# Performance work log

Measured on AMD Instinct MI355X. Metric: run time of the kernel, lower is better.

The kernel has to match this reference:

```python
import jax, jax.numpy as jnp
import numpy as np

B, T, C, FFN, N_LAYER, LAYER_ID = 4, 2048, 1024, 4096, 24, 1
EPS = 1e-5


def setup_inputs() -> dict:
    key = jax.random.key(0)
    ks = jax.random.split(key, 10)
    scale = 0.02

    def w(k, shape):
        return (jax.random.normal(k, shape, jnp.float32) * scale)

    # RWKV-4 init formulas for layer_id=1, n_layer=24 (learned params, init per source)
    r01 = LAYER_ID / (N_LAYER - 1)
    r10 = 1.0 - LAYER_ID / N_LAYER
    ddd = np.arange(C, dtype=np.float64) / C
    h = np.arange(C, dtype=np.float64)
    decay = -5.0 + 8.0 * (h / (C - 1)) ** (0.7 + 1.3 * r01)
    zigzag = np.array([(i + 1) % 3 - 1 for i in range(C)], dtype=np.float64) * 0.5
    tfirst = np.log(0.3) + zigzag

    return {
        "x": jax.random.normal(ks[0], (B, T, C), jnp.float32),
        "ln1_w": jnp.ones((C,), jnp.float32), "ln1_b": jnp.zeros((C,), jnp.float32),
        "ln2_w": jnp.ones((C,), jnp.float32), "ln2_b": jnp.zeros((C,), jnp.float32),
        "time_decay": jnp.asarray(decay, jnp.float32),
        "time_first": jnp.asarray(tfirst, jnp.float32),
        "tmk": jnp.asarray(ddd ** r10, jnp.float32),
        "tmv": jnp.asarray(ddd ** r10 + 0.3 * r01, jnp.float32),
        "tmr": jnp.asarray(ddd ** (0.5 * r10), jnp.float32),
        "att_kw": w(ks[1], (C, C)), "att_vw": w(ks[2], (C, C)),
        "att_rw": w(ks[3], (C, C)), "att_ow": w(ks[4], (C, C)),
        "f_tmk": jnp.asarray(ddd ** r10, jnp.float32),
        "f_tmr": jnp.asarray(ddd ** r10, jnp.float32),
        "f_kw": w(ks[5], (FFN, C)), "f_rw": w(ks[6], (C, C)), "f_vw": w(ks[7], (C, FFN)),
    }


def _ln(z, g, b):
    m = jnp.mean(z, axis=-1, keepdims=True)
    v = jnp.mean(jnp.square(z - m), axis=-1, keepdims=True)
    return (z - m) * jax.lax.rsqrt(v + EPS) * g + b


def _shift(z):  # token shift: prepend zero row along T, drop last
    return jnp.pad(z, ((0, 0), (1, 0), (0, 0)))[:, :-1]


def _wkv(time_decay, u, k, v):
    # Numerically-stable RWKV-4 WKV recurrence (log-space max trick).
    # k, v: [B, T, C]; time_decay, u: [C]
    w = -jnp.exp(time_decay)  # per-channel decay (negative)
    kt = jnp.moveaxis(k, 1, 0)  # [T, B, C]
    vt = jnp.moveaxis(v, 1, 0)
    aa = jnp.zeros_like(kt[0])
    bb = jnp.zeros_like(kt[0])
    pp = jnp.full_like(kt[0], -1e38)

    def step(carry, kv):
        aa, bb, pp = carry
        kk, vv = kv
        ww = u + kk
        p = jnp.maximum(pp, ww)
        e1 = jnp.exp(pp - p)
        e2 = jnp.exp(ww - p)
        out = (e1 * aa + e2 * vv) / (e1 * bb + e2)
        ww2 = pp + w
        p2 = jnp.maximum(ww2, kk)
        e1b = jnp.exp(ww2 - p2)
        e2b = jnp.exp(kk - p2)
        return (e1b * aa + e2b * vv, e1b * bb + e2b, p2), out

    _, out = jax.lax.scan(step, (aa, bb, pp), (kt, vt))
    return jnp.moveaxis(out, 0, 1)  # [B, T, C]


def reference(x, ln1_w, ln1_b, ln2_w, ln2_b, time_decay, time_first,
              tmk, tmv, tmr, att_kw, att_vw, att_rw, att_ow,
              f_tmk, f_tmr, f_kw, f_rw, f_vw):
    # --- RWKV_TimeMix (layer_id != 0; protectors are identity in fwd for finite vals) ---
    h = _ln(x, ln1_w, ln1_b)
    hx = _shift(h)
    xk = h * tmk + hx * (1.0 - tmk)
    xv = h * tmv + hx * (1.0 - tmv)
    xr = h * tmr + hx * (1.0 - tmr)
    k = jnp.einsum('btc,dc->btd', xk, att_kw)
    v = jnp.einsum('btc,dc->btd', xv, att_vw)
    sr = jax.nn.sigmoid(jnp.einsum('btc,dc->btd', xr, att_rw))
    rwkv = sr * _wkv(time_decay, time_first, k, v)
    x = x + jnp.einsum('btd,cd->btc', rwkv, att_ow)
    # --- RWKV_ChannelMix ---
    h = _ln(x, ln2_w, ln2_b)
    hx = _shift(h)
    xk = h * f_tmk + hx * (1.0 - f_tmk)
    xr = h * f_tmr + hx * (1.0 - f_tmr)
    kk = jnp.square(jax.nn.relu(jnp.einsum('btc,fc->btf', xk, f_kw)))
    kv = jnp.einsum('btf,cf->btc', kk, f_vw)
    x = x + jax.nn.sigmoid(jnp.einsum('btc,dc->btd', xr, f_rw)) * kv
    return x
```

## Files before the change

kernel.cpp:

```cpp
#include <hip/hip_runtime.h>
#include <cstdint>

#define C_DIM 1024
#define T_DIM 2048
#define B_DIM 4
#define FFN_DIM 4096
#define NROWS (B_DIM * T_DIM)
#define NELEM ((size_t)NROWS * C_DIM)
#define MB ((size_t)1 << 20)
#define NSEG 32
#define SEGL (T_DIM / NSEG)

typedef __bf16 bf16;
typedef __bf16 bf16x4 __attribute__((ext_vector_type(4)));
typedef __bf16 bf16x8 __attribute__((ext_vector_type(8)));
typedef float  floatx4 __attribute__((ext_vector_type(4)));

#define GLDS(g, l) __builtin_amdgcn_global_load_lds(                          \
    (const __attribute__((address_space(1))) void*)(g),                       \
    (__attribute__((address_space(3))) void*)(l), 16, 0, 0)

__device__ __forceinline__ void store_out(float* p, float v) { *p = v; }
__device__ __forceinline__ void store_out(bf16* p, float v)  { *p = (bf16)v; }

struct W7 {
    const float* s[7];
    bf16*        d[7];
    int          cum[8];
};

__global__ __launch_bounds__(256) void f2b7_kernel(W7 w)
{
    int id = blockIdx.x * 256 + threadIdx.x;
    int seg = 0;
#pragma unroll
    for (int j = 1; j < 7; ++j) if (id >= w.cum[j]) seg = j;
    int i = id - w.cum[seg];
    float4 v = ((const float4*)w.s[seg])[i];
    bf16x4 o = { (bf16)v.x, (bf16)v.y, (bf16)v.z, (bf16)v.w };
    ((bf16x4*)w.d[seg])[i] = o;
}

template<bool HASV>
__global__ __launch_bounds__(256) void lnmix_kernel(const float* __restrict__ x,
                                                    const float* __restrict__ g,
                                                    const float* __restrict__ b,
                                                    const float* __restrict__ mk,
                                                    const float* __restrict__ mv,
                                                    const float* __restrict__ mr,
                                                    bf16* __restrict__ xk,
                                                    bf16* __restrict__ xv,
                                                    bf16* __restrict__ xr)
{
    int row = blockIdx.x;
    int t   = row & (T_DIM - 1);
    int tid = threadIdx.x;
    size_t i4 = (size_t)row * 256 + tid;

    float4 v  = ((const float4*)x)[i4];
    float4 vp = make_float4(0.f, 0.f, 0.f, 0.f);
    if (t != 0) vp = ((const float4*)x)[i4 - 256];

    float s   = v.x + v.y + v.z + v.w;
    float s2  = v.x * v.x + v.y * v.y + v.z * v.z + v.w * v.w;
    float sp  = vp.x + vp.y + vp.z + vp.w;
    float sp2 = vp.x * vp.x + vp.y * vp.y + vp.z * vp.z + vp.w * vp.w;
    for (int off = 32; off > 0; off >>= 1) {
        s   += __shfl_down(s,   off);
        s2  += __shfl_down(s2,  off);
        sp  += __shfl_down(sp,  off);
        sp2 += __shfl_down(sp2, off);
    }
    __shared__ float red[16];
    int lane = tid & 63, wid = tid >> 6;
    if (lane == 0) { red[wid] = s; red[4 + wid] = s2; red[8 + wid] = sp; red[12 + wid] = sp2; }
    __syncthreads();
    s   = red[0] + red[1] + red[2] + red[3];
    s2  = red[4] + red[5] + red[6] + red[7];
    sp  = red[8] + red[9] + red[10] + red[11];
    sp2 = red[12] + red[13] + red[14] + red[15];

    float mean  = s * (1.0f / C_DIM);
    float inv   = rsqrtf(s2 * (1.0f / C_DIM) - mean * mean + 1e-5f);
    float meanp = sp * (1.0f / C_DIM);
    float invp  = rsqrtf(sp2 * (1.0f / C_DIM) - meanp * meanp + 1e-5f);

    float4 gv = ((const float4*)g)[tid];
    float4 bv = ((const float4*)b)[tid];
    float4 hv, hp;
    hv.x = (v.x - mean) * inv * gv.x + bv.x;
    hv.y = (v.y - mean) * inv * gv.y + bv.y;
    hv.z = (v.z - mean) * inv * gv.z + bv.z;
    hv.w = (v.w - mean) * inv * gv.w + bv.w;
    if (t != 0) {
        hp.x = (vp.x - meanp) * invp * gv.x + bv.x;
        hp.y = (vp.y - meanp) * invp * gv.y + bv.y;
        hp.z = (vp.z - meanp) * invp * gv.z + bv.z;
        hp.w = (vp.w - meanp) * invp * gv.w + bv.w;
    } else {
        hp = make_float4(0.f, 0.f, 0.f, 0.f);
    }

    float4 m1 = ((const float4*)mk)[tid];
    bf16x4 o;
    o.x = (bf16)(hp.x + m1.x * (hv.x - hp.x));
    o.y = (bf16)(hp.y + m1.y * (hv.y - hp.y));
    o.z = (bf16)(hp.z + m1.z * (hv.z - hp.z));
    o.w = (bf16)(hp.w + m1.w * (hv.w - hp.w));
    ((bf16x4*)xk)[i4] = o;

    if (HASV) {
        float4 m2 = ((const float4*)mv)[tid];
        o.x = (bf16)(hp.x + m2.x * (hv.x - hp.x));
        o.y = (bf16)(hp.y + m2.y * (hv.y - hp.y));
        o.z = (bf16)(hp.z + m2.z * (hv.z - hp.z));
        o.w = (bf16)(hp.w + m2.w * (hv.w - hp.w));
        ((bf16x4*)xv)[i4] = o;
    }

    float4 m3 = ((const float4*)mr)[tid];
    o.x = (bf16)(hp.x + m3.x * (hv.x - hp.x));
    o.y = (bf16)(hp.y + m3.y * (hv.y - hp.y));
    o.z = (bf16)(hp.z + m3.z * (hv.z - hp.z));
    o.w = (bf16)(hp.w + m3.w * (hv.w - hp.w));
    ((bf16x4*)xr)[i4] = o;
}

#define EPI_NONE 0
#define EPI_SIG 1
#define EPI_RELU2 2
#define EPI_ADD 3
#define EPI_SCALEADD 4

template<int EPI, typename OutT>
__global__ __launch_bounds__(256) void gemm_bf16(const bf16* __restrict__ A,
                                                 const bf16* __restrict__ W,
                                                 OutT* __restrict__ Y,
                                                 const float* __restrict__ X2,
                                                 const bf16* __restrict__ S,
                                                 int N, int K)
{
    __shared__ unsigned short As[128 * 32];
    __shared__ unsigned short Bs[128 * 32];

    int tid = threadIdx.x;
    int ntn    = N >> 7;
    int stride = ntn >> 3;
    int id  = blockIdx.x;
    int sq  = id >> 3;
    int n_t = (id & 7) * stride + (sq % stride);
    int m_t = sq / stride;
    int m0 = m_t * 128, n0 = n_t * 128;

    int r0  = tid >> 2;
    int qsw = ((tid & 3) - ((r0 >> 1) & 3)) & 3;
    const bf16* Ag = A + (size_t)(m0 + r0) * K + qsw * 8;
    const bf16* Wg = W + (size_t)(n0 + r0) * K + qsw * 8;
    size_t rowK = (size_t)64 * K;
    int wv = tid >> 6;
    unsigned short* AsW0 = As + wv * 512;
    unsigned short* AsW1 = As + 2048 + wv * 512;
    unsigned short* BsW0 = Bs + wv * 512;
    unsigned short* BsW1 = Bs + 2048 + wv * 512;

    int ln = tid & 63;
    int wm = (wv & 1) * 64, wn = (wv >> 1) * 64;
    int ra0 = wm + (ln & 15);
    int rb0 = wn + (ln & 15);
    int qa  = ln >> 4;
    int abase = ra0 * 32 + (((qa + (ra0 >> 1)) & 3) * 8);
    int bbase = rb0 * 32 + (((qa + (rb0 >> 1)) & 3) * 8);

    floatx4 acc[4][4] = {};

    for (int k0 = 0; k0 < K; k0 += 32) {
        if (k0) __syncthreads();
        GLDS(Ag + k0,        AsW0);
        GLDS(Ag + k0 + rowK, AsW1);
        GLDS(Wg + k0,        BsW0);
        GLDS(Wg + k0 + rowK, BsW1);
        __syncthreads();

        bf16x8 a[4], b[4];
#pragma unroll
        for (int i = 0; i < 4; ++i) a[i] = *(const bf16x8*)(As + abase + i * 512);
#pragma unroll
        for (int j = 0; j < 4; ++j) b[j] = *(const bf16x8*)(Bs + bbase + j * 512);
#pragma unroll
        for (int i = 0; i < 4; ++i)
#pragma unroll
            for (int j = 0; j < 4; ++j)
                acc[i][j] = __builtin_amdgcn_mfma_f32_16x16x32_bf16(a[i], b[j], acc[i][j], 0, 0, 0);
    }

    int row0 = (ln >> 4) * 4;
    int colb = n0 + wn + (ln & 15);
#pragma unroll
    for (int i = 0; i < 4; ++i) {
        int gm = m0 + wm + i * 16 + row0;
#pragma unroll
        for (int j = 0; j < 4; ++j) {
            int gn = colb + j * 16;
#pragma unroll
            for (int r = 0; r < 4; ++r) {
                size_t idx = (size_t)(gm + r) * N + gn;
                float v = acc[i][j][r];
                if (EPI == EPI_SIG)        v = 1.0f / (1.0f + __expf(-v));
                else if (EPI == EPI_RELU2) { float t = fmaxf(v, 0.0f); v = t * t; }
                else if (EPI == EPI_ADD)   v = X2[idx] + v;
                else if (EPI == EPI_SCALEADD) v = X2[idx] + (float)S[idx] * v;
                store_out(&Y[idx], v);
            }
        }
    }
}

__global__ __launch_bounds__(256) void wkv_seg(const float* __restrict__ k,
                                               const float* __restrict__ v,
                                               const float* __restrict__ decay,
                                               float* __restrict__ sa,
                                               float* __restrict__ sb,
                                               float* __restrict__ sp)
{
    int idx = blockIdx.x * 256 + threadIdx.x;
    int c   = idx & (C_DIM - 1);
    int bs  = idx >> 10;
    int seg = bs & (NSEG - 1);
    int b   = bs >> 5;
    float w = -__expf(decay[c]);
    size_t base = ((size_t)b * T_DIM + (size_t)seg * SEGL) * C_DIM + c;
    float aa = 0.f, bb = 0.f, pp = -1e38f;
    for (int t = 0; t < SEGL; ++t) {
        size_t off = base + (size_t)t * C_DIM;
        float kk = k[off], vv = v[off];
        float ww2 = pp + w;
        float p2  = fmaxf(ww2, kk);
        float e1  = __expf(ww2 - p2);
        float e2  = __expf(kk - p2);
        aa = e1 * aa + e2 * vv;
        bb = e1 * bb + e2;
        pp = p2;
    }
    sa[idx] = aa; sb[idx] = bb; sp[idx] = pp;
}

__global__ __launch_bounds__(256) void wkv_comb(const float* __restrict__ sa,
                                                const float* __restrict__ sb,
                                                const float* __restrict__ sp,
                                                const float* __restrict__ decay,
                                                float* __restrict__ ia,
                                                float* __restrict__ ib,
                                                float* __restrict__ ip)
{
    int idx = blockIdx.x * 256 + threadIdx.x;
    int c = idx & (C_DIM - 1);
    int b = idx >> 10;
    float wL = -__expf(decay[c]) * (float)SEGL;
    float aa = 0.f, bb = 0.f, pp = -1e38f;
    size_t base = (size_t)b * NSEG * C_DIM + c;
    for (int j = 0; j < NSEG; ++j) {
        size_t o = base + (size_t)j * C_DIM;
        ia[o] = aa; ib[o] = bb; ip[o] = pp;
        float a_s = sa[o], b_s = sb[o], p_s = sp[o];
        float pd = pp + wL;
        float pn = fmaxf(pd, p_s);
        float e1 = __expf(pd - pn);
        float e2 = __expf(p_s - pn);
        aa = e1 * aa + e2 * a_s;
        bb = e1 * bb + e2 * b_s;
        pp = pn;
    }
}

__global__ __launch_bounds__(256) void wkv_out(const float* __restrict__ k,
                                               const float* __restrict__ v,
                                               const bf16* __restrict__ sr,
                                               const float* __restrict__ decay,
                                               const float* __restrict__ first,
                                               const float* __restrict__ ia,
                                               const float* __restrict__ ib,
                                               const float* __restrict__ ip,
                                               bf16* __restrict__ out)
{
    int idx = blockIdx.x * 256 + threadIdx.x;
    int c   = idx & (C_DIM - 1);
    int bs  = idx >> 10;
    int seg = bs & (NSEG - 1);
    int b   = bs >> 5;
    float w = -__expf(decay[c]);
    float u = first[c];
    float aa = ia[idx], bb = ib[idx], pp = ip[idx];
    size_t base = ((size_t)b * T_DIM + (size_t)seg * SEGL) * C_DIM + c;
    for (int t = 0; t < SEGL; ++t) {
        size_t off = base + (size_t)t * C_DIM;
        float kk = k[off], vv = v[off];
        float ww = u + kk;
        float p  = fmaxf(pp, ww);
        float e1 = __expf(pp - p);
        float e2 = __expf(ww - p);
        float o  = (e1 * aa + e2 * vv) / (e1 * bb + e2);
        out[off] = (bf16)((float)sr[off] * o);
        float ww2 = pp + w;
        float p2  = fmaxf(ww2, kk);
        float e1b = __expf(ww2 - p2);
        float e2b = __expf(kk - p2);
        aa = e1b * aa + e2b * vv;
        bb = e1b * bb + e2b;
        pp = p2;
    }
}

extern "C" void kernel_launch(void* const* d_in, const int* in_sizes, int n_in,
                              void* d_out, int out_size, void* d_ws, size_t ws_size,
                              hipStream_t stream)
{
    const float* x          = (const float*)d_in[0];
    const float* ln1_w      = (const float*)d_in[1];
    const float* ln1_b      = (const float*)d_in[2];
    const float* ln2_w      = (const float*)d_in[3];
    const float* ln2_b      = (const float*)d_in[4];
    const float* time_decay = (const float*)d_in[5];
    const float* time_first = (const float*)d_in[6];
    const float* tmk        = (const float*)d_in[7];
    const float* tmv        = (const float*)d_in[8];
    const float* tmr        = (const float*)d_in[9];
    const float* att_kw     = (const float*)d_in[10];
    const float* att_vw     = (const float*)d_in[11];
    const float* att_rw     = (const float*)d_in[12];
    const float* att_ow     = (const float*)d_in[13];
    const float* f_tmk      = (const float*)d_in[14];
    const float* f_tmr      = (const float*)d_in[15];
    const float* f_kw       = (const float*)d_in[16];
    const float* f_rw       = (const float*)d_in[17];
    const float* f_vw       = (const float*)d_in[18];
    float* out = (float*)d_out;

    char* W8 = (char*)d_ws;
    bf16* kw_b  = (bf16*)(W8 + 0 * MB);
    bf16* vw_b  = (bf16*)(W8 + 2 * MB);
    bf16* rw_b  = (bf16*)(W8 + 4 * MB);
    bf16* ow_b  = (bf16*)(W8 + 6 * MB);
    bf16* fkw_b = (bf16*)(W8 + 8 * MB);
    bf16* frw_b = (bf16*)(W8 + 16 * MB);
    bf16* fvw_b = (bf16*)(W8 + 18 * MB);

    bf16*  xk_b   = (bf16*)(W8 + 26 * MB);
    bf16*  xv_b   = (bf16*)(W8 + 42 * MB);
    bf16*  xr_b   = (bf16*)(W8 + 58 * MB);
    bf16*  rwkv_b = xk_b;
    bf16*  xk2_b  = (bf16*)(W8 + 26 * MB);
    bf16*  xr2_b  = (bf16*)(W8 + 42 * MB);
    bf16*  sr2_b  = (bf16*)(W8 + 58 * MB);
    float* kbuf   = (float*)(W8 + 74 * MB);
    float* vbuf   = (float*)(W8 + 106 * MB);
    bf16*  srb_b  = (bf16*)(W8 + 138 * MB);
    bf16*  kk_b   = (bf16*)(W8 + 106 * MB);

    size_t KB512 = (size_t)512 * 1024;
    float* sc_a = (float*)(W8 + 170 * MB);
    float* sc_b = (float*)(W8 + 170 * MB + 1 * KB512);
    float* sc_p = (float*)(W8 + 170 * MB + 2 * KB512);
    float* in_a = (float*)(W8 + 170 * MB + 3 * KB512);
    float* in_b = (float*)(W8 + 170 * MB + 4 * KB512);
    float* in_p = (float*)(W8 + 170 * MB + 5 * KB512);

    int nC4 = C_DIM * C_DIM / 4, nF4 = FFN_DIM * C_DIM / 4;
    W7 w7;
    const float* srcs[7] = { att_kw, att_vw, att_rw, att_ow, f_kw, f_rw, f_vw };
    bf16*        dsts[7] = { kw_b, vw_b, rw_b, ow_b, fkw_b, frw_b, fvw_b };
    int          cnts[7] = { nC4, nC4, nC4, nC4, nF4, nC4, nF4 };
    int cum = 0;
    for (int i = 0; i < 7; ++i) { w7.s[i] = srcs[i]; w7.d[i] = dsts[i]; w7.cum[i] = cum; cum += cnts[i]; }
    w7.cum[7] = cum;
    f2b7_kernel<<<cum / 256, 256, 0, stream>>>(w7);

    dim3 gC(8 * 64);
    dim3 gF(32 * 64);
    int segGrid = B_DIM * NSEG * C_DIM / 256;

    lnmix_kernel<true><<<NROWS, 256, 0, stream>>>(x, ln1_w, ln1_b, tmk, tmv, tmr,
                                                  xk_b, xv_b, xr_b);
    gemm_bf16<EPI_NONE, float><<<gC, 256, 0, stream>>>(xk_b, kw_b, kbuf, nullptr, nullptr, C_DIM, C_DIM);
    gemm_bf16<EPI_NONE, float><<<gC, 256, 0, stream>>>(xv_b, vw_b, vbuf, nullptr, nullptr, C_DIM, C_DIM);
    gemm_bf16<EPI_SIG,  bf16 ><<<gC, 256, 0, stream>>>(xr_b, rw_b, srb_b, nullptr, nullptr, C_DIM, C_DIM);
    wkv_seg<<<segGrid, 256, 0, stream>>>(kbuf, vbuf, time_decay, sc_a, sc_b, sc_p);
    wkv_comb<<<B_DIM * C_DIM / 256, 256, 0, stream>>>(sc_a, sc_b, sc_p, time_decay, in_a, in_b, in_p);
    wkv_out<<<segGrid, 256, 0, stream>>>(kbuf, vbuf, srb_b, time_decay, time_first,
                                         in_a, in_b, in_p, rwkv_b);
    gemm_bf16<EPI_ADD,  float><<<gC, 256, 0, stream>>>(rwkv_b, ow_b, out, x, nullptr, C_DIM, C_DIM);

    lnmix_kernel<false><<<NROWS, 256, 0, stream>>>(out, ln2_w, ln2_b, f_tmk, nullptr, f_tmr,
                                                   xk2_b, nullptr, xr2_b);
    gemm_bf16<EPI_SIG,   bf16><<<gC, 256, 0, stream>>>(xr2_b, frw_b, sr2_b, nullptr, nullptr, C_DIM, C_DIM);
    gemm_bf16<EPI_RELU2, bf16><<<gF, 256, 0, stream>>>(xk2_b, fkw_b, kk_b, nullptr, nullptr, FFN_DIM, C_DIM);
    gemm_bf16<EPI_SCALEADD, float><<<gC, 256, 0, stream>>>(kk_b, fvw_b, out, out, sr2_b, C_DIM, FFN_DIM);
}
```

Measured before the change: 560.3 us.

## Batch independent GEMMs into grouped launches and use narrower tiles for C-output GEMMs

Replaces the templated per-GEMM kernel with a grouped kernel that takes up to three problems in one launch, so the K/V/R projections share a single launch, as do the FFN key and receptance projections. The output-projection and FFN value GEMMs move to 128x64 tiles, which doubles their block count for better CU occupancy. The aim is to cut launch overhead and tail effects from small grids. In exchange, the epilogue type and output format are now chosen with runtime branches instead of being fixed at compile time, and the smaller tiles reuse the A operand less.

```diff
diff --git a/kernel.cpp b/kernel.cpp
--- a/kernel.cpp
+++ b/kernel.cpp
@@ -19,9 +19,6 @@
 #define GLDS(g, l) __builtin_amdgcn_global_load_lds(                          \
     (const __attribute__((address_space(1))) void*)(g),                       \
     (__attribute__((address_space(3))) void*)(l), 16, 0, 0)
-
-__device__ __forceinline__ void store_out(float* p, float v) { *p = v; }
-__device__ __forceinline__ void store_out(bf16* p, float v)  { *p = (bf16)v; }
 
 struct W7 {
     const float* s[7];
@@ -132,64 +129,84 @@
 #define EPI_ADD 3
 #define EPI_SCALEADD 4
 
-template<int EPI, typename OutT>
-__global__ __launch_bounds__(256) void gemm_bf16(const bf16* __restrict__ A,
-                                                 const bf16* __restrict__ W,
-                                                 OutT* __restrict__ Y,
-                                                 const float* __restrict__ X2,
-                                                 const bf16* __restrict__ S,
-                                                 int N, int K)
-{
+struct GemmProb {
+    const bf16* A;
+    const bf16* W;
+    void*       Y;
+    const float* X2;
+    const bf16*  S;
+    int N, K, epi, outBf16;
+};
+struct GemmBatch {
+    GemmProb p[3];
+    int cum[4];
+};
+
+template<int BN>
+__global__ __launch_bounds__(256) void gemm_bat(GemmBatch bat)
+{
+    constexpr int NJ = BN / 32;
     __shared__ unsigned short As[128 * 32];
-    __shared__ unsigned short Bs[128 * 32];
+    __shared__ unsigned short Bs[BN * 32];
 
     int tid = threadIdx.x;
-    int ntn    = N >> 7;
+    int id  = blockIdx.x;
+    int pi  = (id >= bat.cum[1]) + (id >= bat.cum[2]);
+    const bf16* PA = bat.p[pi].A;
+    const bf16* PW = bat.p[pi].W;
+    void*       PY = bat.p[pi].Y;
+    const float* PX2 = bat.p[pi].X2;
+    const bf16*  PS  = bat.p[pi].S;
+    int N = bat.p[pi].N, K = bat.p[pi].K;
+    int epi = bat.p[pi].epi, obf = bat.p[pi].outBf16;
+    int lid = id - bat.cum[pi];
+
+    int ntn    = N / BN;
     int stride = ntn >> 3;
-    int id  = blockIdx.x;
-    int sq  = id >> 3;
-    int n_t = (id & 7) * stride + (sq % stride);
-    int m_t = sq / stride;
-    int m0 = m_t * 128, n0 = n_t * 128;
+    int sh     = __ffs(stride) - 1;
+    int sq  = lid >> 3;
+    int n_t = (lid & 7) * stride + (sq & (stride - 1));
+    int m_t = sq >> sh;
+    int m0 = m_t * 128, n0 = n_t * BN;
 
     int r0  = tid >> 2;
     int qsw = ((tid & 3) - ((r0 >> 1) & 3)) & 3;
-    const bf16* Ag = A + (size_t)(m0 + r0) * K + qsw * 8;
-    const bf16* Wg = W + (size_t)(n0 + r0) * K + qsw * 8;
+    const bf16* Ag = PA + (size_t)(m0 + r0) * K + qsw * 8;
+    const bf16* Wg = PW + (size_t)(n0 + r0) * K + qsw * 8;
     size_t rowK = (size_t)64 * K;
     int wv = tid >> 6;
     unsigned short* AsW0 = As + wv * 512;
     unsigned short* AsW1 = As + 2048 + wv * 512;
     unsigned short* BsW0 = Bs + wv * 512;
-    unsigned short* BsW1 = Bs + 2048 + wv * 512;
+    unsigned short* BsW1 = Bs + (BN == 128 ? 2048 : 0) + wv * 512;
 
     int ln = tid & 63;
-    int wm = (wv & 1) * 64, wn = (wv >> 1) * 64;
+    int wm = (wv & 1) * 64, wn = (wv >> 1) * (BN / 2);
     int ra0 = wm + (ln & 15);
     int rb0 = wn + (ln & 15);
     int qa  = ln >> 4;
     int abase = ra0 * 32 + (((qa + (ra0 >> 1)) & 3) * 8);
     int bbase = rb0 * 32 + (((qa + (rb0 >> 1)) & 3) * 8);
 
-    floatx4 acc[4][4] = {};
+    floatx4 acc[4][NJ] = {};
 
     for (int k0 = 0; k0 < K; k0 += 32) {
         if (k0) __syncthreads();
         GLDS(Ag + k0,        AsW0);
         GLDS(Ag + k0 + rowK, AsW1);
         GLDS(Wg + k0,        BsW0);
-        GLDS(Wg + k0 + rowK, BsW1);
+        if constexpr (BN == 128) GLDS(Wg + k0 + rowK, BsW1);
         __syncthreads();
 
-        bf16x8 a[4], b[4];
+        bf16x8 a[4], b[NJ];
 #pragma unroll
         for (int i = 0; i < 4; ++i) a[i] = *(const bf16x8*)(As + abase + i * 512);
 #pragma unroll
-        for (int j = 0; j < 4; ++j) b[j] = *(const bf16x8*)(Bs + bbase + j * 512);
+        for (int j = 0; j < NJ; ++j) b[j] = *(const bf16x8*)(Bs + bbase + j * 512);
 #pragma unroll
         for (int i = 0; i < 4; ++i)
 #pragma unroll
-            for (int j = 0; j < 4; ++j)
+            for (int j = 0; j < NJ; ++j)
                 acc[i][j] = __builtin_amdgcn_mfma_f32_16x16x32_bf16(a[i], b[j], acc[i][j], 0, 0, 0);
     }
 
@@ -199,17 +216,18 @@
     for (int i = 0; i < 4; ++i) {
         int gm = m0 + wm + i * 16 + row0;
 #pragma unroll
-        for (int j = 0; j < 4; ++j) {
+        for (int j = 0; j < NJ; ++j) {
             int gn = colb + j * 16;
 #pragma unroll
             for (int r = 0; r < 4; ++r) {
                 size_t idx = (size_t)(gm + r) * N + gn;
                 float v = acc[i][j][r];
-                if (EPI == EPI_SIG)        v = 1.0f / (1.0f + __expf(-v));
-                else if (EPI == EPI_RELU2) { float t = fmaxf(v, 0.0f); v = t * t; }
-                else if (EPI == EPI_ADD)   v = X2[idx] + v;
-                else if (EPI == EPI_SCALEADD) v = X2[idx] + (float)S[idx] * v;
-                store_out(&Y[idx], v);
+                if (epi == EPI_SIG)        v = 1.0f / (1.0f + __expf(-v));
+                else if (epi == EPI_RELU2) { float t2 = fmaxf(v, 0.0f); v = t2 * t2; }
+                else if (epi == EPI_ADD)   v = PX2[idx] + v;
+                else if (epi == EPI_SCALEADD) v = PX2[idx] + (float)PS[idx] * v;
+                if (obf) ((bf16*)PY)[idx] = (bf16)v;
+                else     ((float*)PY)[idx] = v;
             }
         }
     }
@@ -374,24 +392,51 @@
     w7.cum[7] = cum;
     f2b7_kernel<<<cum / 256, 256, 0, stream>>>(w7);
 
-    dim3 gC(8 * 64);
-    dim3 gF(32 * 64);
     int segGrid = B_DIM * NSEG * C_DIM / 256;
+
+    auto prob = [](const bf16* A, const bf16* W, void* Y, const float* X2,
+                   const bf16* S, int N, int K, int epi, int obf) {
+        GemmProb p; p.A = A; p.W = W; p.Y = Y; p.X2 = X2; p.S = S;
+        p.N = N; p.K = K; p.epi = epi; p.outBf16 = obf; return p;
+    };
 
     lnmix_kernel<true><<<NROWS, 256, 0, stream>>>(x, ln1_w, ln1_b, tmk, tmv, tmr,
                                                   xk_b, xv_b, xr_b);
-    gemm_bf16<EPI_NONE, float><<<gC, 256, 0, stream>>>(xk_b, kw_b, kbuf, nullptr, nullptr, C_DIM, C_DIM);
-    gemm_bf16<EPI_NONE, float><<<gC, 256, 0, stream>>>(xv_b, vw_b, vbuf, nullptr, nullptr, C_DIM, C_DIM);
-    gemm_bf16<EPI_SIG,  bf16 ><<<gC, 256, 0, stream>>>(xr_b, rw_b, srb_b, nullptr, nullptr, C_DIM, C_DIM);
+    {
+        GemmBatch b3;
+        b3.p[0] = prob(xk_b, kw_b, kbuf,  nullptr, nullptr, C_DIM, C_DIM, EPI_NONE, 0);
+        b3.p[1] = prob(xv_b, vw_b, vbuf,  nullptr, nullptr, C_DIM, C_DIM, EPI_NONE, 0);
+        b3.p[2] = prob(xr_b, rw_b, srb_b, nullptr, nullptr, C_DIM, C_DIM, EPI_SIG,  1);
+        b3.cum[0] = 0; b3.cum[1] = 512; b3.cum[2] = 1024; b3.cum[3] = 1536;
+        gemm_bat<128><<<1536, 256, 0, stream>>>(b3);
+    }
     wkv_seg<<<segGrid, 256, 0, stream>>>(kbuf, vbuf, time_decay, sc_a, sc_b, sc_p);
     wkv_comb<<<B_DIM * C_DIM / 256, 256, 0, stream>>>(sc_a, sc_b, sc_p, time_decay, in_a, in_b, in_p);
     wkv_out<<<segGrid, 256, 0, stream>>>(kbuf, vbuf, srb_b, time_decay, time_first,
                                          in_a, in_b, in_p, rwkv_b);
-    gemm_bf16<EPI_ADD,  float><<<gC, 256, 0, stream>>>(rwkv_b, ow_b, out, x, nullptr, C_DIM, C_DIM);
+    {
+        GemmBatch b1;
+        b1.p[0] = prob(rwkv_b, ow_b, out, x, nullptr, C_DIM, C_DIM, EPI_ADD, 0);
+        b1.p[1] = b1.p[0]; b1.p[2] = b1.p[0];
+        b1.cum[0] = 0; b1.cum[1] = 1024; b1.cum[2] = 1024; b1.cum[3] = 1024;
+        gemm_bat<64><<<1024, 256, 0, stream>>>(b1);
+    }
 
     lnmix_kernel<false><<<NROWS, 256, 0, stream>>>(out, ln2_w, ln2_b, f_tmk, nullptr, f_tmr,
                                                    xk2_b, nullptr, xr2_b);
-    gemm_bf16<EPI_SIG,   bf16><<<gC, 256, 0, stream>>>(xr2_b, frw_b, sr2_b, nullptr, nullptr, C_DIM, C_DIM);
-    gemm_bf16<EPI_RELU2, bf16><<<gF, 256, 0, stream>>>(xk2_b, fkw_b, kk_b, nullptr, nullptr, FFN_DIM, C_DIM);
-    gemm_bf16<EPI_SCALEADD, float><<<gC, 256, 0, stream>>>(kk_b, fvw_b, out, out, sr2_b, C_DIM, FFN_DIM);
-}
+    {
+        GemmBatch b2;
+        b2.p[0] = prob(xk2_b, fkw_b, kk_b,  nullptr, nullptr, FFN_DIM, C_DIM, EPI_RELU2, 1);
+        b2.p[1] = prob(xr2_b, frw_b, sr2_b, nullptr, nullptr, C_DIM,   C_DIM, EPI_SIG,   1);
+        b2.p[2] = b2.p[1];
+        b2.cum[0] = 0; b2.cum[1] = 2048; b2.cum[2] = 2560; b2.cum[3] = 2560;
+        gemm_bat<128><<<2560, 256, 0, stream>>>(b2);
+    }
+    {
+        GemmBatch b1;
+        b1.p[0] = prob(kk_b, fvw_b, out, out, sr2_b, C_DIM, FFN_DIM, EPI_SCALEADD, 0);
+        b1.p[1] = b1.p[0]; b1.p[2] = b1.p[0];
+        b1.cum[0] = 0; b1.cum[1] = 1024; b1.cum[2] = 1024; b1.cum[3] = 1024;
+        gemm_bat<64><<<1024, 256, 0, stream>>>(b1);
+    }
+}
```

Measured after the change: 580.9 us. 3.7% more time.
